# Optimization experiments

Hardware: AMD Instinct MI355X
Metric: run time of the kernel (lower is better)

Reference implementation:

```python
import jax, jax.numpy as jnp
import numpy as np

H = 768      # hidden_size
NH = 12      # num_attention_heads
HD = H // NH # head_dim = 64
EPS = 1e-5


def setup_inputs() -> dict:
    key = jax.random.key(0)
    ks = jax.random.split(key, 12)
    B, S = 2, 2048
    s = 1.0 / np.sqrt(H)
    return {
        "hidden_states": jax.random.normal(ks[0], (B, S, H), dtype=jnp.float32),
        "attention_mask": jax.random.normal(ks[1], (B, S), dtype=jnp.float32),
        "Wq": jax.random.normal(ks[2], (H, H), dtype=jnp.float32) * s,
        "bq": jnp.zeros((H,), dtype=jnp.float32),
        "Wk": jax.random.normal(ks[3], (H, H), dtype=jnp.float32) * s,
        "bk": jnp.zeros((H,), dtype=jnp.float32),
        "Wv": jax.random.normal(ks[4], (H, H), dtype=jnp.float32) * s,
        "bv": jnp.zeros((H,), dtype=jnp.float32),
        "Wo": jax.random.normal(ks[5], (H, H), dtype=jnp.float32) * s,
        "bo": jnp.zeros((H,), dtype=jnp.float32),
        "ln_gamma": jnp.ones((H,), dtype=jnp.float32),
        "ln_beta": jnp.zeros((H,), dtype=jnp.float32),
    }


def reference(hidden_states, attention_mask, Wq, bq, Wk, bk, Wv, bv, Wo, bo, ln_gamma, ln_beta):
    B, S, E = hidden_states.shape
    # QKV projections -> [B, NH, S, HD]
    def proj(W, b):
        return (hidden_states @ W + b).reshape(B, S, NH, HD).transpose(0, 2, 1, 3)
    q = proj(Wq, bq)
    k = proj(Wk, bk)
    v = proj(Wv, bv)
    # scores [B, NH, S, S]
    att = jnp.einsum('bhqd,bhkd->bhqk', q, k) * (1.0 / np.sqrt(HD))
    # padding pair mask: valid iff mask>=0 at both query and key positions
    valid = (attention_mask >= 0)  # [B, S]
    pair = valid[:, None, :, None] & valid[:, None, None, :]  # [B,1,S,S]
    att = jnp.where(pair, att, -1e9)
    att = jax.nn.softmax(att, axis=-1)
    # dropout p=0 (eval) -> identity
    ctx = jnp.einsum('bhqk,bhkd->bhqd', att, v)  # [B,NH,S,HD]
    ctx = ctx.transpose(0, 2, 1, 3).reshape(B, S, E)
    # output dense + residual + LayerNorm
    h = ctx @ Wo + bo + hidden_states
    mu = jnp.mean(h, axis=-1, keepdims=True)
    var = jnp.mean(jnp.square(h - mu), axis=-1, keepdims=True)
    out = (h - mu) * jax.lax.rsqrt(var + EPS) * ln_gamma + ln_beta
    return out
```

## Files before the change

kernel.cpp:

```cpp
#include <hip/hip_runtime.h>
#include <hip/hip_bf16.h>

#define H_DIM 768
#define NHEAD 12
#define HDIM  64
#define S_LEN 2048
#define B_SZ  2
#define M_TOT (B_SZ * S_LEN)
#define NQKV  (3 * H_DIM)
#define LN_EPS 1e-5f
#define SM_C   0.1803368801f

typedef __attribute__((ext_vector_type(8))) short bf16x8;
typedef __attribute__((ext_vector_type(4))) float f32x4;

static __device__ inline ushort f2bf(float x) {
    __hip_bfloat16 h = __float2bfloat16(x);
    ushort u;
    __builtin_memcpy(&u, &h, 2);
    return u;
}
static __device__ inline float bf2f(ushort u) {
    unsigned int v = ((unsigned int)u) << 16;
    float f;
    __builtin_memcpy(&f, &v, 4);
    return f;
}

#define GLDS16(g, l) __builtin_amdgcn_global_load_lds( \
    (const __attribute__((address_space(1))) void*)(g), \
    (__attribute__((address_space(3))) void*)(l), 16, 0, 0)

__global__ __launch_bounds__(256)
void prep(const float* __restrict__ hs,
          const float* __restrict__ Wq, const float* __restrict__ Wk,
          const float* __restrict__ Wv, const float* __restrict__ Wo,
          const float* __restrict__ bq, const float* __restrict__ bk,
          const float* __restrict__ bv,
          ushort* __restrict__ Xbf, ushort* __restrict__ Wcat,
          ushort* __restrict__ Wot, float* __restrict__ bcat)
{
    __shared__ ushort T[64][65];
    const int bid = blockIdx.x;
    const int t   = threadIdx.x;

    if (bid < 3072) {
        const int i = (bid * 256 + t) * 4;
        f32x4 v = *(const f32x4*)(hs + i);
        ushort4 o;
        o.x = f2bf(v[0]); o.y = f2bf(v[1]); o.z = f2bf(v[2]); o.w = f2bf(v[3]);
        *(ushort4*)(Xbf + i) = o;
    } else if (bid < 3072 + 576) {
        const int bid2 = bid - 3072;
        const int z = bid2 / 144;
        const int rem = bid2 % 144;
        const int n0 = (rem / 12) * 64;
        const int k0 = (rem % 12) * 64;
        const float* W = (z == 0) ? Wq : (z == 1) ? Wk : (z == 2) ? Wv : Wo;
        const int r = t >> 2, c0 = (t & 3) * 16;
        const float* src = W + (size_t)(k0 + r) * H_DIM + n0 + c0;
        #pragma unroll
        for (int j = 0; j < 16; j += 4) {
            f32x4 v = *(const f32x4*)(src + j);
            #pragma unroll
            for (int jj = 0; jj < 4; ++jj) T[r][c0 + j + jj] = f2bf(v[jj]);
        }
        __syncthreads();
        bf16x8 o0, o1;
        #pragma unroll
        for (int j = 0; j < 8; ++j) {
            o0[j] = (short)T[c0 + j][r];
            o1[j] = (short)T[c0 + 8 + j][r];
        }
        ushort* dst = (z < 3)
            ? Wcat + (size_t)(z * 768 + n0 + r) * H_DIM + k0 + c0
            : Wot  + (size_t)(n0 + r) * H_DIM + k0 + c0;
        *(bf16x8*)dst       = o0;
        *(bf16x8*)(dst + 8) = o1;
    } else {
        const int i = (bid - 3648) * 256 + t;
        if (i < NQKV) {
            float v = (i < 768) ? bq[i] : (i < 1536) ? bk[i - 768] : bv[i - 1536];
            bcat[i] = v;
        }
    }
}

template<int OUTMODE>
__global__ __launch_bounds__(256)
void gemm_mfma(const ushort* __restrict__ A, const ushort* __restrict__ Bt,
               const float* __restrict__ bias, const float* __restrict__ resid,
               void* __restrict__ outp, ushort* __restrict__ vtp,
               int M, int N, int K, int nscale, float sfac)
{
    __shared__ ushort As[128 * 32];
    __shared__ ushort Bs[128 * 32];
    const int bn = blockIdx.x * 128;
    const int bm = blockIdx.y * 128;
    const int t  = threadIdx.x;
    const int w  = t >> 6, l = t & 63;
    const int lg = l >> 4, lr = l & 15;
    const int wr = w >> 1, wc = w & 1;

    f32x4 acc[4][4];
    #pragma unroll
    for (int i = 0; i < 4; ++i)
        #pragma unroll
        for (int j = 0; j < 4; ++j) acc[i][j] = (f32x4){0.f, 0.f, 0.f, 0.f};

    for (int k0 = 0; k0 < K; k0 += 32) {
        #pragma unroll
        for (int it = 0; it < 2; ++it) {
            const int g = it * 256 + t;
            const int r = g >> 2, cb = (g & 3) * 8;
            GLDS16(A  + (size_t)(bm + r) * K + k0 + cb, (char*)As + g * 16);
            GLDS16(Bt + (size_t)(bn + r) * K + k0 + cb, (char*)Bs + g * 16);
        }
        __syncthreads();
        bf16x8 af[4], bfr[4];
        #pragma unroll
        for (int m16 = 0; m16 < 4; ++m16)
            af[m16] = *(const bf16x8*)&As[(wr * 64 + m16 * 16 + lr) * 32 + lg * 8];
        #pragma unroll
        for (int n16 = 0; n16 < 4; ++n16)
            bfr[n16] = *(const bf16x8*)&Bs[(wc * 64 + n16 * 16 + lr) * 32 + lg * 8];
        #pragma unroll
        for (int m16 = 0; m16 < 4; ++m16)
            #pragma unroll
            for (int n16 = 0; n16 < 4; ++n16)
                acc[m16][n16] = __builtin_amdgcn_mfma_f32_16x16x32_bf16(
                    af[m16], bfr[n16], acc[m16][n16], 0, 0, 0);
        __syncthreads();
    }

    #pragma unroll
    for (int m16 = 0; m16 < 4; ++m16) {
        #pragma unroll
        for (int n16 = 0; n16 < 4; ++n16) {
            const int col = bn + wc * 64 + n16 * 16 + lr;
            const float bcol = bias[col];
            const int row0 = bm + wr * 64 + m16 * 16 + lg * 4;
            float vv[4];
            #pragma unroll
            for (int r = 0; r < 4; ++r) {
                float v = acc[m16][n16][r] + bcol;
                if (OUTMODE == 1) v += resid[(size_t)(row0 + r) * N + col];
                else if (col < nscale) v *= sfac;
                vv[r] = v;
            }
            if (OUTMODE == 1) {
                #pragma unroll
                for (int r = 0; r < 4; ++r)
                    ((float*)outp)[(size_t)(row0 + r) * N + col] = vv[r];
            } else if (col >= 1536) {
                const int dfull = col - 1536;
                const int hh = dfull >> 6, dd = dfull & 63;
                const int bb = row0 >> 11, ss = row0 & 2047;
                ushort4 pk;
                pk.x = f2bf(vv[0]); pk.y = f2bf(vv[1]);
                pk.z = f2bf(vv[2]); pk.w = f2bf(vv[3]);
                *(ushort4*)(vtp + ((size_t)(bb * NHEAD + hh) * HDIM + dd) * S_LEN + ss) = pk;
            } else {
                #pragma unroll
                for (int r = 0; r < 4; ++r)
                    ((ushort*)outp)[(size_t)(row0 + r) * N + col] = f2bf(vv[r]);
            }
        }
    }
}

#define KT     64
#define ATT_QT 128
#define KVHALF (S_LEN / 2)
#define NTILES (KVHALF / KT)

__global__ __launch_bounds__(256, 3)
void attn_mfma(const ushort* __restrict__ Qbf, const ushort* __restrict__ Kbf,
               const ushort* __restrict__ Vt, const float* __restrict__ mask,
               ushort* __restrict__ Pp, float* __restrict__ lp)
{
    const int qt = blockIdx.x, h = blockIdx.y;
    const int b  = blockIdx.z >> 1, half = blockIdx.z & 1;
    const int t  = threadIdx.x;
    const int w  = t >> 6, l = t & 63;
    const int lg = l >> 4, lr = l & 15;
    const int q0 = qt * ATT_QT;
    const int kb0 = half * KVHALF;

    __shared__ ushort Ks[3][KT][64];
    __shared__ ushort Vs[2][HDIM][64];
    __shared__ ushort Ps[4][16][64];
    __shared__ float  kmarg[KVHALF];

    {
        const int i = t * 4;
        f32x4 v = *(const f32x4*)(mask + b * S_LEN + kb0 + i);
        #pragma unroll
        for (int j = 0; j < 4; ++j)
            kmarg[i + j] = (v[j] >= 0.f) ? 0.f : -1e30f;
    }

    bool qn[2][4];
    #pragma unroll
    for (int qg = 0; qg < 2; ++qg)
        #pragma unroll
        for (int r = 0; r < 4; ++r)
            qn[qg][r] = (mask[b * S_LEN + q0 + w * 32 + qg * 16 + lg * 4 + r] < 0.f);

    bf16x8 qa[2][2];
    #pragma unroll
    for (int qg = 0; qg < 2; ++qg) {
        const ushort* qsrc = Qbf
            + (size_t)(b * S_LEN + q0 + w * 32 + qg * 16 + lr) * NQKV
            + h * HDIM + lg * 8;
        qa[qg][0] = *(const bf16x8*)qsrc;
        qa[qg][1] = *(const bf16x8*)(qsrc + 32);
    }

    const int srow = w * 16 + (l >> 3);
    const int scol = ((l & 7) ^ (l >> 3)) * 8;
    const ushort* kLane = Kbf + (size_t)(b * S_LEN + kb0 + srow) * NQKV
                        + h * HDIM + scol;
    const ushort* vLane = Vt + ((size_t)(b * NHEAD + h) * HDIM + srow) * S_LEN
                        + kb0 + scol;
    char* ldsK = (char*)Ks + w * 2048 + l * 16;
    char* ldsV = (char*)Vs + w * 2048 + l * 16;

    __syncthreads();

    GLDS16(kLane, ldsK);
    GLDS16(kLane + (size_t)8 * NQKV, ldsK + 1024);
    GLDS16(vLane, ldsV);
    GLDS16(vLane + (size_t)8 * S_LEN, ldsV + 1024);
    GLDS16(kLane + (size_t)KT * NQKV, ldsK + 8192);
    GLDS16(kLane + (size_t)(KT + 8) * NQKV, ldsK + 8192 + 1024);

    float l_r[2][4] = {{0.f,0.f,0.f,0.f},{0.f,0.f,0.f,0.f}};
    f32x4 accO[2][4];
    #pragma unroll
    for (int qg = 0; qg < 2; ++qg)
        #pragma unroll
        for (int ct = 0; ct < 4; ++ct) accO[qg][ct] = (f32x4){0.f,0.f,0.f,0.f};

    const int  swz = (lr & 7) << 4;
    char* PsW = (char*)Ps + w * 2048;

    for (int tt = 0; tt < NTILES; ++tt) {
        if (tt < NTILES - 1) {
            asm volatile("s_waitcnt vmcnt(2)" ::: "memory");
        } else {
            asm volatile("s_waitcnt vmcnt(0)" ::: "memory");
        }
        __builtin_amdgcn_s_barrier();

        if (tt + 1 < NTILES) {
            const ushort* vsrc = vLane + (size_t)(tt + 1) * KT;
            char* lv = ldsV + ((tt + 1) & 1) * 8192;
            GLDS16(vsrc, lv);
            GLDS16(vsrc + (size_t)8 * S_LEN, lv + 1024);
            if (tt + 2 < NTILES) {
                const ushort* ksrc = kLane + (size_t)(tt + 2) * KT * NQKV;
                char* lk = ldsK + ((tt + 2) % 3) * 8192;
                GLDS16(ksrc, lk);
                GLDS16(ksrc + (size_t)8 * NQKV, lk + 1024);
            }
        }

        const char* Kc = (const char*)Ks + (tt % 3) * 8192;
        const char* Vc = (const char*)Vs + (tt & 1) * 8192;

        float karr[4];
        #pragma unroll
        for (int ct = 0; ct < 4; ++ct)
            karr[ct] = kmarg[tt * KT + 16 * ct + lr];

        f32x4 sc[2][4];
        __builtin_amdgcn_s_setprio(1);
        #pragma unroll
        for (int ct = 0; ct < 4; ++ct) {
            bf16x8 bk0 = *(const bf16x8*)(Kc + (16 * ct + lr) * 128 + ((lg * 16) ^ swz));
            bf16x8 bk1 = *(const bf16x8*)(Kc + (16 * ct + lr) * 128 + ((lg * 16 + 64) ^ swz));
            #pragma unroll
            for (int qg = 0; qg < 2; ++qg) {
                f32x4 a = __builtin_amdgcn_mfma_f32_16x16x32_bf16(
                    qa[qg][0], bk0, (f32x4){0.f,0.f,0.f,0.f}, 0, 0, 0);
                sc[qg][ct] = __builtin_amdgcn_mfma_f32_16x16x32_bf16(
                    qa[qg][1], bk1, a, 0, 0, 0);
            }
        }
        __builtin_amdgcn_s_setprio(0);

        bf16x8 bv[4][2];
        #pragma unroll
        for (int ct = 0; ct < 4; ++ct) {
            bv[ct][0] = *(const bf16x8*)(Vc + (16 * ct + lr) * 128 + ((lg * 16) ^ swz));
            bv[ct][1] = *(const bf16x8*)(Vc + (16 * ct + lr) * 128 + ((lg * 16 + 64) ^ swz));
        }

        #pragma unroll
        for (int qg = 0; qg < 2; ++qg) {
            #pragma unroll
            for (int r = 0; r < 4; ++r) {
                const int qrow = lg * 4 + r;
                const int qsw  = (qrow & 7) << 4;
                #pragma unroll
                for (int ct = 0; ct < 4; ++ct) {
                    float arg = sc[qg][ct][r] + karr[ct];
                    arg = qn[qg][r] ? 0.f : arg;
                    const float p = exp2f(arg);
                    l_r[qg][r] += p;
                    *(ushort*)(PsW + qrow * 128 + ((32 * ct + 2 * lr) ^ qsw)) = f2bf(p);
                }
            }
            __builtin_amdgcn_s_setprio(1);
            #pragma unroll
            for (int kvb = 0; kvb < 2; ++kvb) {
                bf16x8 pa = *(const bf16x8*)(PsW + lr * 128
                                             + ((lg * 16 + kvb * 64) ^ swz));
                #pragma unroll
                for (int ct = 0; ct < 4; ++ct)
                    accO[qg][ct] = __builtin_amdgcn_mfma_f32_16x16x32_bf16(
                        pa, bv[ct][kvb], accO[qg][ct], 0, 0, 0);
            }
            __builtin_amdgcn_s_setprio(0);
        }
    }

    #pragma unroll
    for (int qg = 0; qg < 2; ++qg)
        #pragma unroll
        for (int r = 0; r < 4; ++r) {
            float s = l_r[qg][r];
            #pragma unroll
            for (int off = 1; off < 16; off <<= 1)
                s += __shfl_xor(s, off, 64);
            l_r[qg][r] = s;
        }

    const size_t MN = (size_t)M_TOT * H_DIM;
    #pragma unroll
    for (int qg = 0; qg < 2; ++qg) {
        #pragma unroll
        for (int r = 0; r < 4; ++r) {
            const int m = b * S_LEN + q0 + w * 32 + qg * 16 + lg * 4 + r;
            const size_t base = (size_t)half * MN + (size_t)m * H_DIM + h * HDIM;
            #pragma unroll
            for (int ct = 0; ct < 4; ++ct)
                Pp[base + 16 * ct + lr] = f2bf(accO[qg][ct][r]);
            if (lr == 0)
                lp[half * (M_TOT * NHEAD) + m * NHEAD + h] = l_r[qg][r];
        }
    }
}

__global__ __launch_bounds__(256)
void combine_kernel(const ushort* __restrict__ Pp, const float* __restrict__ lp,
                    ushort* __restrict__ ctx)
{
    const int idx = blockIdx.x * 256 + threadIdx.x;
    const int m  = idx / 96;
    const int c8 = idx % 96;
    const int c  = c8 * 8;
    const int h  = c8 >> 3;
    const size_t MN = (size_t)M_TOT * H_DIM;

    const float lsum = lp[m * NHEAD + h] + lp[M_TOT * NHEAD + m * NHEAD + h];
    const float inv  = 1.0f / lsum;

    bf16x8 a = *(const bf16x8*)(Pp + (size_t)m * H_DIM + c);
    bf16x8 b = *(const bf16x8*)(Pp + MN + (size_t)m * H_DIM + c);
    bf16x8 o;
    #pragma unroll
    for (int j = 0; j < 8; ++j)
        o[j] = (short)f2bf((bf2f((ushort)a[j]) + bf2f((ushort)b[j])) * inv);
    *(bf16x8*)(ctx + (size_t)m * H_DIM + c) = o;
}

__global__ __launch_bounds__(256)
void ln_kernel(const float* __restrict__ Hbuf, const float* __restrict__ gamma,
               const float* __restrict__ beta, float* __restrict__ out)
{
    const int m = blockIdx.x * 4 + (threadIdx.x >> 6);
    const int l = threadIdx.x & 63;
    const float* row = Hbuf + (size_t)m * H_DIM;

    f32x4 x[3];
    #pragma unroll
    for (int k = 0; k < 3; ++k) x[k] = *(const f32x4*)(row + l * 4 + k * 256);

    float s = 0.f;
    #pragma unroll
    for (int k = 0; k < 3; ++k)
        #pragma unroll
        for (int j = 0; j < 4; ++j) s += x[k][j];
    #pragma unroll
    for (int off = 1; off < 64; off <<= 1) s += __shfl_xor(s, off, 64);
    const float mu = s * (1.0f / H_DIM);

    float v = 0.f;
    #pragma unroll
    for (int k = 0; k < 3; ++k)
        #pragma unroll
        for (int j = 0; j < 4; ++j) {
            const float d = x[k][j] - mu;
            v += d * d;
        }
    #pragma unroll
    for (int off = 1; off < 64; off <<= 1) v += __shfl_xor(v, off, 64);
    const float rstd = rsqrtf(v * (1.0f / H_DIM) + LN_EPS);

    #pragma unroll
    for (int k = 0; k < 3; ++k) {
        const int c = l * 4 + k * 256;
        f32x4 gm = *(const f32x4*)(gamma + c);
        f32x4 bt = *(const f32x4*)(beta + c);
        f32x4 o;
        #pragma unroll
        for (int j = 0; j < 4; ++j)
            o[j] = (x[k][j] - mu) * rstd * gm[j] + bt[j];
        *(f32x4*)(out + (size_t)m * H_DIM + c) = o;
    }
}

extern "C" void kernel_launch(void* const* d_in, const int* in_sizes, int n_in,
                              void* d_out, int out_size, void* d_ws, size_t ws_size,
                              hipStream_t stream)
{
    const float* hs   = (const float*)d_in[0];
    const float* mask = (const float*)d_in[1];
    const float* Wq   = (const float*)d_in[2];
    const float* bq   = (const float*)d_in[3];
    const float* Wk   = (const float*)d_in[4];
    const float* bk   = (const float*)d_in[5];
    const float* Wv   = (const float*)d_in[6];
    const float* bv   = (const float*)d_in[7];
    const float* Wo   = (const float*)d_in[8];
    const float* bo   = (const float*)d_in[9];
    const float* g    = (const float*)d_in[10];
    const float* be   = (const float*)d_in[11];
    float* out = (float*)d_out;

    char* base = (char*)d_ws;
    ushort* Xbf    = (ushort*)(base);
    ushort* QKVbf  = (ushort*)(base + 6291456);
    ushort* Wcat   = (ushort*)(base + 25165824);
    ushort* Wot    = (ushort*)(base + 28704768);
    float*  bcat   = (float*) (base + 29884416);
    ushort* Vt     = (ushort*)(base + 29893632);
    ushort* Cbf    = (ushort*)(base + 36185088);
    float*  Hb     = (float*) (base + 42476544);
    float*  lp     = (float*) (base + 25165824);
    ushort* Pp     = (ushort*)(base + 42476544);

    prep<<<3657, 256, 0, stream>>>(hs, Wq, Wk, Wv, Wo, bq, bk, bv,
                                   Xbf, Wcat, Wot, bcat);

    gemm_mfma<0><<<dim3(NQKV / 128, M_TOT / 128), 256, 0, stream>>>(
        Xbf, Wcat, bcat, nullptr, QKVbf, Vt, M_TOT, NQKV, H_DIM, 768, SM_C);

    attn_mfma<<<dim3(S_LEN / ATT_QT, NHEAD, B_SZ * 2), 256, 0, stream>>>(
        QKVbf, QKVbf + 768, Vt, mask, Pp, lp);

    combine_kernel<<<M_TOT * 96 / 256, 256, 0, stream>>>(Pp, lp, Cbf);

    gemm_mfma<1><<<dim3(H_DIM / 128, M_TOT / 128), 256, 0, stream>>>(
        Cbf, Wot, bo, hs, Hb, nullptr, M_TOT, H_DIM, H_DIM, 0, 1.0f);

    ln_kernel<<<M_TOT / 4, 256, 0, stream>>>(Hb, g, be, out);
}
```

Before: 128.7 us.

## Use 32x32x16 MFMA with transposed scores to keep P in registers

Rewrites the attention inner loop to compute S^T (K as the A operand, Q as B) with 32x32x16 bf16 MFMAs, so each lane holds a full query column of probabilities. The probabilities are packed directly into the A operand for the PV MFMA, which removes the per-wave LDS staging buffer for P along with its write/read round trip. Row sums reduce to a single cross-half shuffle. In exchange, V fragments are now gathered with two 8-byte LDS reads each, and the larger accumulators change register pressure, which may affect occupancy at the three-blocks-per-CU launch bound.

```diff
diff --git a/kernel.cpp b/kernel.cpp
--- a/kernel.cpp
+++ b/kernel.cpp
@@ -11,8 +11,11 @@
 #define LN_EPS 1e-5f
 #define SM_C   0.1803368801f
 
-typedef __attribute__((ext_vector_type(8))) short bf16x8;
-typedef __attribute__((ext_vector_type(4))) float f32x4;
+typedef __attribute__((ext_vector_type(8)))  short bf16x8;
+typedef __attribute__((ext_vector_type(4)))  float f32x4;
+typedef __attribute__((ext_vector_type(16))) float f32x16;
+typedef __attribute__((ext_vector_type(4)))  int   i32x4;
+typedef __attribute__((ext_vector_type(2)))  int   i32x2;
 
 static __device__ inline ushort f2bf(float x) {
     __hip_bfloat16 h = __float2bfloat16(x);
@@ -25,6 +28,9 @@
     float f;
     __builtin_memcpy(&f, &v, 4);
     return f;
+}
+static __device__ inline unsigned pack2bf(float lo, float hi) {
+    return (unsigned)f2bf(lo) | ((unsigned)f2bf(hi) << 16);
 }
 
 #define GLDS16(g, l) __builtin_amdgcn_global_load_lds( \
@@ -183,13 +189,12 @@
     const int b  = blockIdx.z >> 1, half = blockIdx.z & 1;
     const int t  = threadIdx.x;
     const int w  = t >> 6, l = t & 63;
-    const int lg = l >> 4, lr = l & 15;
+    const int l31 = l & 31, hi = l >> 5;
     const int q0 = qt * ATT_QT;
     const int kb0 = half * KVHALF;
 
     __shared__ ushort Ks[3][KT][64];
     __shared__ ushort Vs[2][HDIM][64];
-    __shared__ ushort Ps[4][16][64];
     __shared__ float  kmarg[KVHALF];
 
     {
@@ -200,21 +205,15 @@
             kmarg[i + j] = (v[j] >= 0.f) ? 0.f : -1e30f;
     }
 
-    bool qn[2][4];
-    #pragma unroll
-    for (int qg = 0; qg < 2; ++qg)
-        #pragma unroll
-        for (int r = 0; r < 4; ++r)
-            qn[qg][r] = (mask[b * S_LEN + q0 + w * 32 + qg * 16 + lg * 4 + r] < 0.f);
-
-    bf16x8 qa[2][2];
-    #pragma unroll
-    for (int qg = 0; qg < 2; ++qg) {
-        const ushort* qsrc = Qbf
-            + (size_t)(b * S_LEN + q0 + w * 32 + qg * 16 + lr) * NQKV
-            + h * HDIM + lg * 8;
-        qa[qg][0] = *(const bf16x8*)qsrc;
-        qa[qg][1] = *(const bf16x8*)(qsrc + 32);
+    const bool qnL = (mask[b * S_LEN + q0 + w * 32 + l31] < 0.f);
+
+    bf16x8 qa[4];
+    {
+        const ushort* qsrc = Qbf + (size_t)(b * S_LEN + q0 + w * 32 + l31) * NQKV
+                           + h * HDIM + 8 * hi;
+        #pragma unroll
+        for (int k = 0; k < 4; ++k)
+            qa[k] = *(const bf16x8*)(qsrc + 16 * k);
     }
 
     const int srow = w * 16 + (l >> 3);
@@ -235,15 +234,14 @@
     GLDS16(kLane + (size_t)KT * NQKV, ldsK + 8192);
     GLDS16(kLane + (size_t)(KT + 8) * NQKV, ldsK + 8192 + 1024);
 
-    float l_r[2][4] = {{0.f,0.f,0.f,0.f},{0.f,0.f,0.f,0.f}};
-    f32x4 accO[2][4];
-    #pragma unroll
-    for (int qg = 0; qg < 2; ++qg)
-        #pragma unroll
-        for (int ct = 0; ct < 4; ++ct) accO[qg][ct] = (f32x4){0.f,0.f,0.f,0.f};
-
-    const int  swz = (lr & 7) << 4;
-    char* PsW = (char*)Ps + w * 2048;
+    float l_part = 0.f;
+    f32x16 accO[2];
+    #pragma unroll
+    for (int dt = 0; dt < 2; ++dt)
+        #pragma unroll
+        for (int i = 0; i < 16; ++i) accO[dt][i] = 0.f;
+
+    const int swzl = (l31 & 7) << 4;
 
     for (int tt = 0; tt < NTILES; ++tt) {
         if (tt < NTILES - 1) {
@@ -269,87 +267,85 @@
         const char* Kc = (const char*)Ks + (tt % 3) * 8192;
         const char* Vc = (const char*)Vs + (tt & 1) * 8192;
 
-        float karr[4];
-        #pragma unroll
-        for (int ct = 0; ct < 4; ++ct)
-            karr[ct] = kmarg[tt * KT + 16 * ct + lr];
-
-        f32x4 sc[2][4];
-        __builtin_amdgcn_s_setprio(1);
-        #pragma unroll
-        for (int ct = 0; ct < 4; ++ct) {
-            bf16x8 bk0 = *(const bf16x8*)(Kc + (16 * ct + lr) * 128 + ((lg * 16) ^ swz));
-            bf16x8 bk1 = *(const bf16x8*)(Kc + (16 * ct + lr) * 128 + ((lg * 16 + 64) ^ swz));
+        #pragma unroll
+        for (int kvt = 0; kvt < 2; ++kvt) {
+            f32x16 sc;
+            __builtin_amdgcn_s_setprio(1);
+            {
+                const char* abase = Kc + (kvt * 32 + l31) * 128;
+                bf16x8 a0 = *(const bf16x8*)(abase + ((16 * hi +  0) ^ swzl));
+                bf16x8 a1 = *(const bf16x8*)(abase + ((16 * hi + 32) ^ swzl));
+                bf16x8 a2 = *(const bf16x8*)(abase + ((16 * hi + 64) ^ swzl));
+                bf16x8 a3 = *(const bf16x8*)(abase + ((16 * hi + 96) ^ swzl));
+                f32x16 z;
+                #pragma unroll
+                for (int i = 0; i < 16; ++i) z[i] = 0.f;
+                sc = __builtin_amdgcn_mfma_f32_32x32x16_bf16(a0, qa[0], z, 0, 0, 0);
+                sc = __builtin_amdgcn_mfma_f32_32x32x16_bf16(a1, qa[1], sc, 0, 0, 0);
+                sc = __builtin_amdgcn_mfma_f32_32x32x16_bf16(a2, qa[2], sc, 0, 0, 0);
+                sc = __builtin_amdgcn_mfma_f32_32x32x16_bf16(a3, qa[3], sc, 0, 0, 0);
+            }
+            __builtin_amdgcn_s_setprio(0);
+
+            float p[16];
+            const float* km = &kmarg[tt * 64 + kvt * 32 + 4 * hi];
             #pragma unroll
-            for (int qg = 0; qg < 2; ++qg) {
-                f32x4 a = __builtin_amdgcn_mfma_f32_16x16x32_bf16(
-                    qa[qg][0], bk0, (f32x4){0.f,0.f,0.f,0.f}, 0, 0, 0);
-                sc[qg][ct] = __builtin_amdgcn_mfma_f32_16x16x32_bf16(
-                    qa[qg][1], bk1, a, 0, 0, 0);
-            }
-        }
-        __builtin_amdgcn_s_setprio(0);
-
-        bf16x8 bv[4][2];
-        #pragma unroll
-        for (int ct = 0; ct < 4; ++ct) {
-            bv[ct][0] = *(const bf16x8*)(Vc + (16 * ct + lr) * 128 + ((lg * 16) ^ swz));
-            bv[ct][1] = *(const bf16x8*)(Vc + (16 * ct + lr) * 128 + ((lg * 16 + 64) ^ swz));
-        }
-
-        #pragma unroll
-        for (int qg = 0; qg < 2; ++qg) {
-            #pragma unroll
-            for (int r = 0; r < 4; ++r) {
-                const int qrow = lg * 4 + r;
-                const int qsw  = (qrow & 7) << 4;
+            for (int q4 = 0; q4 < 4; ++q4) {
+                f32x4 kq = *(const f32x4*)(km + 8 * q4);
                 #pragma unroll
-                for (int ct = 0; ct < 4; ++ct) {
-                    float arg = sc[qg][ct][r] + karr[ct];
-                    arg = qn[qg][r] ? 0.f : arg;
-                    const float p = exp2f(arg);
-                    l_r[qg][r] += p;
-                    *(ushort*)(PsW + qrow * 128 + ((32 * ct + 2 * lr) ^ qsw)) = f2bf(p);
+                for (int r = 0; r < 4; ++r) {
+                    float arg = sc[q4 * 4 + r] + kq[r];
+                    arg = qnL ? 0.f : arg;
+                    const float pv = exp2f(arg);
+                    p[q4 * 4 + r] = pv;
+                    l_part += pv;
                 }
             }
+
             __builtin_amdgcn_s_setprio(1);
             #pragma unroll
-            for (int kvb = 0; kvb < 2; ++kvb) {
-                bf16x8 pa = *(const bf16x8*)(PsW + lr * 128
-                                             + ((lg * 16 + kvb * 64) ^ swz));
+            for (int cc = 0; cc < 2; ++cc) {
+                i32x4 pku;
+                pku[0] = (int)pack2bf(p[8 * cc + 0], p[8 * cc + 1]);
+                pku[1] = (int)pack2bf(p[8 * cc + 2], p[8 * cc + 3]);
+                pku[2] = (int)pack2bf(p[8 * cc + 4], p[8 * cc + 5]);
+                pku[3] = (int)pack2bf(p[8 * cc + 6], p[8 * cc + 7]);
+                bf16x8 pa;
+                __builtin_memcpy(&pa, &pku, 16);
+                const int c = kvt * 2 + cc;
                 #pragma unroll
-                for (int ct = 0; ct < 4; ++ct)
-                    accO[qg][ct] = __builtin_amdgcn_mfma_f32_16x16x32_bf16(
-                        pa, bv[ct][kvb], accO[qg][ct], 0, 0, 0);
+                for (int dt = 0; dt < 2; ++dt) {
+                    const char* vrow = Vc + (32 * dt + l31) * 128;
+                    i32x2 v0 = *(const i32x2*)(vrow + ((32 * c + 8 * hi) ^ swzl));
+                    i32x2 v1 = *(const i32x2*)(vrow + ((32 * c + 16 + 8 * hi) ^ swzl));
+                    i32x4 vv;
+                    vv[0] = v0[0]; vv[1] = v0[1]; vv[2] = v1[0]; vv[3] = v1[1];
+                    bf16x8 bv;
+                    __builtin_memcpy(&bv, &vv, 16);
+                    accO[dt] = __builtin_amdgcn_mfma_f32_32x32x16_bf16(
+                        pa, bv, accO[dt], 0, 0, 0);
+                }
             }
             __builtin_amdgcn_s_setprio(0);
         }
     }
 
-    #pragma unroll
-    for (int qg = 0; qg < 2; ++qg)
-        #pragma unroll
-        for (int r = 0; r < 4; ++r) {
-            float s = l_r[qg][r];
-            #pragma unroll
-            for (int off = 1; off < 16; off <<= 1)
-                s += __shfl_xor(s, off, 64);
-            l_r[qg][r] = s;
-        }
+    l_part += __shfl_xor(l_part, 32, 64);
 
     const size_t MN = (size_t)M_TOT * H_DIM;
     #pragma unroll
-    for (int qg = 0; qg < 2; ++qg) {
-        #pragma unroll
-        for (int r = 0; r < 4; ++r) {
-            const int m = b * S_LEN + q0 + w * 32 + qg * 16 + lg * 4 + r;
-            const size_t base = (size_t)half * MN + (size_t)m * H_DIM + h * HDIM;
-            #pragma unroll
-            for (int ct = 0; ct < 4; ++ct)
-                Pp[base + 16 * ct + lr] = f2bf(accO[qg][ct][r]);
-            if (lr == 0)
-                lp[half * (M_TOT * NHEAD) + m * NHEAD + h] = l_r[qg][r];
-        }
+    for (int dt = 0; dt < 2; ++dt) {
+        #pragma unroll
+        for (int reg = 0; reg < 16; ++reg) {
+            const int q = (reg & 3) + 8 * (reg >> 2) + 4 * hi;
+            const int m = b * S_LEN + q0 + w * 32 + q;
+            Pp[(size_t)half * MN + (size_t)m * H_DIM + h * HDIM + 32 * dt + l31]
+                = f2bf(accO[dt][reg]);
+        }
+    }
+    if (hi == 0) {
+        const int m = b * S_LEN + q0 + w * 32 + l31;
+        lp[half * (M_TOT * NHEAD) + m * NHEAD + h] = l_part;
     }
 }
 
```

After: 125.6 us. 2.4% less time.
